# Optimization experiments

Hardware: AMD Instinct MI355X
Metric: run time of the kernel (lower is better)

Reference implementation:

```python
import jax, jax.numpy as jnp
import numpy as np

NUM_NODES = 50000
NUM_EDGES = 800000
NUM_REL = 8
DIM = 64
NUM_BLOCKS = 8


def setup_inputs() -> dict:
    key = jax.random.key(0)
    ks = jax.random.split(key, 6)
    x = jax.random.normal(ks[0], (NUM_NODES, DIM), dtype=jnp.float32)
    source = jax.random.randint(ks[1], (NUM_EDGES,), 0, NUM_NODES)
    target = jax.random.randint(ks[2], (NUM_EDGES,), 0, NUM_NODES)
    edge_type = jax.random.randint(ks[3], (NUM_EDGES,), 0, NUM_REL)
    edge_weights = jax.random.uniform(ks[4], (NUM_EDGES,), dtype=jnp.float32)
    bs = DIM // NUM_BLOCKS
    # xavier_normal_ for (bs, bs) blocks: std = sqrt(2 / (fan_in + fan_out))
    std = (2.0 / (bs + bs)) ** 0.5
    blocks = std * jax.random.normal(ks[5], (NUM_REL, NUM_BLOCKS, bs, bs), dtype=jnp.float32)
    return {
        "x": x,
        "blocks": blocks,
        "edge_weights": edge_weights,
        "source": source,
        "target": target,
        "edge_type": edge_type,
    }


def reference(x, blocks, edge_weights, source, target, edge_type):
    # input_dim == output_dim -> use_horizontal_stacking is False -> vertically stacked path.
    # Vertically stacked adjacency: adj[(edge_type * N + target), source] = edge_weights,
    # so (adj @ x) is a per-(relation,target) scatter-add of weighted source features.
    n = x.shape[0]
    r, b, ib, ob = blocks.shape
    seg = edge_type * n + target                               # (E,) row index in stacked adj
    msgs = x[source] * edge_weights[:, None]                   # (E, in_dim)
    agg = jax.ops.segment_sum(msgs, seg, num_segments=r * n)   # (R*N, in_dim)
    agg = agg.reshape(r, n, b, ib)                             # (R, N, B, ib)
    out = jnp.einsum("rbio,rnbi->nbo", blocks, agg)            # sum over relations + block matmul
    return out.reshape(n, b * ob)                              # (N, out_dim)
```

## Files before the change

kernel.cpp:

```cpp
#include <hip/hip_runtime.h>


#define DIM 64
#define NBLK 8
#define BS 8
#define NREL 8
#define COL_PAD 12
#define LDS_T_TOTAL (NREL * NBLK * BS * COL_PAD)
#define CHUNK 64

#define TILE 4096
#define MAXB 1024
#define SORTW_CAP 4096

typedef unsigned int uint32;
typedef unsigned long long uint64;
typedef unsigned short uint16;

__global__ __launch_bounds__(512) void histA(
    const int* __restrict__ tgt, uint32* __restrict__ tile_hist,
    int num_edges, int nb)
{
    __shared__ uint32 h[MAXB];
    for (int i = threadIdx.x; i < nb; i += 512) h[i] = 0u;
    __syncthreads();
    const int base = blockIdx.x * TILE;
    const int end  = min(base + TILE, num_edges);
    for (int j = base + (int)threadIdx.x; j < end; j += 512)
        atomicAdd(&h[tgt[j] >> 6], 1u);
    __syncthreads();
    uint32* dst = tile_hist + (size_t)blockIdx.x * nb;
    for (int i = threadIdx.x; i < nb; i += 512) dst[i] = h[i];
}

__global__ __launch_bounds__(64) void colscan(
    uint32* __restrict__ tile_hist, uint32* __restrict__ totals,
    int nt, int nb)
{
    const int b    = blockIdx.x;
    const int lane = threadIdx.x;
    uint32 carry = 0;
    for (int t0 = 0; t0 < nt; t0 += 64) {
        const int t = t0 + lane;
        uint32 v = (t < nt) ? tile_hist[(size_t)t * nb + b] : 0u;
        uint32 xin = v;
#pragma unroll
        for (int d = 1; d < 64; d <<= 1) {
            uint32 tm = __shfl_up(xin, d, 64);
            if (lane >= d) xin += tm;
        }
        if (t < nt) tile_hist[(size_t)t * nb + b] = carry + xin - v;
        carry += __shfl(xin, 63, 64);
    }
    if (lane == 0) totals[b] = carry;
}

__global__ __launch_bounds__(512) void scan_totals(
    const uint32* __restrict__ totals, uint32* __restrict__ bbase, int nb)
{
    __shared__ uint32 wtot[8];
    const int tid = threadIdx.x, lane = tid & 63, wid = tid >> 6;
    uint32 carry = 0;
    const int nch = (nb + 511) >> 9;
    for (int c = 0; c < nch; ++c) {
        const int idx = (c << 9) + tid;
        uint32 v = (idx < nb) ? totals[idx] : 0u;
        uint32 xin = v;
#pragma unroll
        for (int d = 1; d < 64; d <<= 1) {
            uint32 t = __shfl_up(xin, d, 64);
            if (lane >= d) xin += t;
        }
        if (lane == 63) wtot[wid] = xin;
        __syncthreads();
        if (wid == 0) {
            uint32 y = (lane < 8) ? wtot[lane] : 0u;
#pragma unroll
            for (int d = 1; d < 8; d <<= 1) {
                uint32 t = __shfl_up(y, d, 64);
                if (lane >= d) y += t;
            }
            if (lane < 8) wtot[lane] = y;
        }
        __syncthreads();
        const uint32 base = carry + ((wid > 0) ? wtot[wid - 1] : 0u);
        if (idx < nb) bbase[idx] = base + xin - v;
        carry += wtot[7];
        __syncthreads();
    }
    if (tid == 0) bbase[nb] = carry;
}

__global__ __launch_bounds__(512) void scatterB(
    const int* __restrict__ src, const int* __restrict__ tgt,
    const int* __restrict__ etype, const float* __restrict__ ew,
    const uint32* __restrict__ tile_hist, const uint32* __restrict__ bbase,
    uint64* __restrict__ payload, int num_edges, int nb)
{
    __shared__ uint32 cur[MAXB];
    const uint32* th = tile_hist + (size_t)blockIdx.x * nb;
    for (int i = threadIdx.x; i < nb; i += 512) cur[i] = bbase[i] + th[i];
    __syncthreads();
    const int base = blockIdx.x * TILE;
    const int end  = min(base + TILE, num_edges);
    for (int j = base + (int)threadIdx.x; j < end; j += 512) {
        const int t = tgt[j];
        const uint32 pos = atomicAdd(&cur[t >> 6], 1u);
        const uint32 lo = (uint32)src[j] | ((uint32)etype[j] << 16)
                        | ((uint32)(t & 63) << 19);
        payload[pos] = ((uint64)__float_as_uint(ew[j]) << 32) | lo;
    }
}

__global__ __launch_bounds__(256) void sortW(
    uint64* __restrict__ payload, uint16* __restrict__ keyt,
    const uint32* __restrict__ bbase)
{
    __shared__ uint64 pay[SORTW_CAP];
    __shared__ uint32 hist[64];
    __shared__ uint32 cur[64];
    const int b   = blockIdx.x;
    const int beg = (int)bbase[b];
    const int cnt = (int)bbase[b + 1] - beg;

    if (cnt > SORTW_CAP) {
        for (int k = threadIdx.x; k < cnt; k += 256) {
            const uint32 lo = (uint32)payload[beg + k];
            keyt[beg + k] = (uint16)((b << 6) | ((lo >> 19) & 63u));
        }
        return;
    }

    for (int k = threadIdx.x; k < cnt; k += 256) pay[k] = payload[beg + k];
    if (threadIdx.x < 64) hist[threadIdx.x] = 0u;
    __syncthreads();
    for (int k = threadIdx.x; k < cnt; k += 256)
        atomicAdd(&hist[((uint32)pay[k] >> 19) & 63u], 1u);
    __syncthreads();
    if (threadIdx.x < 64) {
        const int lane = threadIdx.x;
        uint32 v = hist[lane], xin = v;
#pragma unroll
        for (int d = 1; d < 64; d <<= 1) {
            uint32 t = __shfl_up(xin, d, 64);
            if (lane >= d) xin += t;
        }
        cur[lane] = xin - v;
    }
    __syncthreads();
    for (int k = threadIdx.x; k < cnt; k += 256) {
        const uint64 p  = pay[k];
        const uint32 tl = ((uint32)p >> 19) & 63u;
        const uint32 pos = atomicAdd(&cur[tl], 1u);
        payload[beg + pos] = p;
        keyt[beg + pos] = (uint16)((b << 6) | tl);
    }
}

#define PRE(i, p_)                                                          \
    const uint32 lo##i = (uint32)(p_);                                      \
    const float  w##i  = __uint_as_float((uint32)((p_) >> 32));             \
    const float* bp##i = bcol + ((lo##i >> 16) & 7) * (NBLK * BS * COL_PAD);\
    const float4 c0_##i = *(const float4*)bp##i;                            \
    const float4 c1_##i = *(const float4*)(bp##i + 4);                      \
    const float4* xs##i = (const float4*)(x + (size_t)(lo##i & 0xFFFF) * DIM + b * BS); \
    const float4 v0_##i = xs##i[0];                                         \
    const float4 v1_##i = xs##i[1];

#define ACC(i, t_)                                                          \
    {                                                                       \
        const int tt = (int)(t_);                                           \
        if (tt != tcur) {                                                   \
            atomicAdd(out + (size_t)tcur * DIM + lane, acc);                \
            acc = 0.0f; tcur = tt;                                          \
        }                                                                   \
        acc = fmaf(w##i,                                                    \
                   v0_##i.x * c0_##i.x + v0_##i.y * c0_##i.y +              \
                   v0_##i.z * c0_##i.z + v0_##i.w * c0_##i.w +              \
                   v1_##i.x * c1_##i.x + v1_##i.y * c1_##i.y +              \
                   v1_##i.z * c1_##i.z + v1_##i.w * c1_##i.w, acc);         \
    }

__global__ __launch_bounds__(512) void rgcn_chunk_kernel(
    const float* __restrict__ x,
    const float* __restrict__ blocks,
    const uint64* __restrict__ payload,
    const uint16* __restrict__ keyt,
    float* __restrict__ out,
    int num_edges)
{
    __shared__ float blkT[LDS_T_TOTAL];
    for (int l = threadIdx.x; l < NREL * NBLK * BS * BS; l += blockDim.x) {
        const int o = l & 7;
        const int i = (l >> 3) & 7;
        const int rb = l >> 6;
        blkT[(rb * 8 + o) * COL_PAD + i] = blocks[l];
    }
    __syncthreads();

    const int lane = threadIdx.x & 63;
    const int wid  = __builtin_amdgcn_readfirstlane(threadIdx.x >> 6);
    const int wave = blockIdx.x * (int)(blockDim.x >> 6) + wid;
    const int beg  = wave * CHUNK;
    if (beg >= num_edges) return;
    const int end  = min(beg + CHUNK, num_edges);

    const int b  = lane >> 3;
    const int oo = lane & 7;
    const float* bcol = &blkT[(b * 8 + oo) * COL_PAD];

    int   tcur = (int)keyt[beg];
    float acc  = 0.0f;

    int j = beg;
    for (; j + 4 <= end; j += 4) {
        const uint64 p0 = payload[j];
        const uint64 p1 = payload[j + 1];
        const uint64 p2 = payload[j + 2];
        const uint64 p3 = payload[j + 3];
        const ushort4 kk = *(const ushort4*)(keyt + j);
        PRE(0, p0) PRE(1, p1) PRE(2, p2) PRE(3, p3)
        ACC(0, kk.x) ACC(1, kk.y) ACC(2, kk.z) ACC(3, kk.w)
    }
    for (; j < end; ++j) {
        const uint64 p0 = payload[j];
        const uint16 k0 = keyt[j];
        PRE(0, p0)
        ACC(0, k0)
    }
    atomicAdd(out + (size_t)tcur * DIM + lane, acc);
}

#define LDS_BLK_STRIDE 72
#define LDS_REL_STRIDE (NBLK * LDS_BLK_STRIDE)
#define LDS_TOTAL (NREL * LDS_REL_STRIDE)

__global__ __launch_bounds__(256) void rgcn_edge_kernel(
    const float* __restrict__ x, const float* __restrict__ blocks,
    const float* __restrict__ ew, const int* __restrict__ src,
    const int* __restrict__ tgt, const int* __restrict__ etype,
    float* __restrict__ out, int num_edges)
{
    __shared__ float blk[LDS_TOTAL];
    for (int l = threadIdx.x; l < NREL * NBLK * BS * BS; l += blockDim.x) {
        int r = l >> 9, bb = (l >> 6) & 7, rest = l & 63;
        blk[r * LDS_REL_STRIDE + bb * LDS_BLK_STRIDE + rest] = blocks[l];
    }
    __syncthreads();
    const int lane = threadIdx.x & 63;
    const int wave = blockIdx.x * (blockDim.x >> 6) + (threadIdx.x >> 6);
    const int total_waves = gridDim.x * (blockDim.x >> 6);
    const int b = lane >> 3;
    for (int e = wave; e < num_edges; e += total_waves) {
        const int s = src[e], t = tgt[e], r = etype[e];
        const float w = ew[e];
        const float4* xs = reinterpret_cast<const float4*>(x + (size_t)s * DIM + b * BS);
        const float4 v0 = xs[0], v1 = xs[1];
        const float* bb = &blk[r * LDS_REL_STRIDE + b * LDS_BLK_STRIDE + (lane & 7)];
        float a = v0.x * bb[0] + v0.y * bb[BS] + v0.z * bb[2 * BS] + v0.w * bb[3 * BS]
                + v1.x * bb[4 * BS] + v1.y * bb[5 * BS] + v1.z * bb[6 * BS] + v1.w * bb[7 * BS];
        atomicAdd(&out[(size_t)t * DIM + lane], w * a);
    }
}

extern "C" void kernel_launch(void* const* d_in, const int* in_sizes, int n_in,
                              void* d_out, int out_size, void* d_ws, size_t ws_size,
                              hipStream_t stream) {
    const float* x      = (const float*)d_in[0];
    const float* blocks = (const float*)d_in[1];
    const float* ew     = (const float*)d_in[2];
    const int*   src    = (const int*)d_in[3];
    const int*   tgt    = (const int*)d_in[4];
    const int*   etype  = (const int*)d_in[5];
    float* out = (float*)d_out;

    const int num_edges = in_sizes[2];
    const int num_nodes = in_sizes[0] / DIM;

    const int nb = (num_nodes + 63) >> 6;
    const int nt = (num_edges + TILE - 1) / TILE;

    const size_t payload_b = (size_t)num_edges * 8;
    const size_t keyt_b    = (size_t)num_edges * 2;
    const size_t th_b      = (size_t)nt * nb * 4;
    const size_t tot_b     = (size_t)nb * 4;
    const size_t bb_b      = (size_t)(nb + 1) * 4;
    const size_t need      = payload_b + keyt_b + th_b + tot_b + bb_b;

    if (nb > MAXB || ws_size < need) {
        hipMemsetAsync(d_out, 0, (size_t)out_size * sizeof(float), stream);
        rgcn_edge_kernel<<<2048, 256, 0, stream>>>(
            x, blocks, ew, src, tgt, etype, out, num_edges);
        return;
    }

    char* ws = (char*)d_ws;
    uint64* payload   = (uint64*)ws;
    uint16* keyt      = (uint16*)(ws + payload_b);
    uint32* tile_hist = (uint32*)(ws + payload_b + keyt_b);
    uint32* totals    = (uint32*)(ws + payload_b + keyt_b + th_b);
    uint32* bbase     = (uint32*)(ws + payload_b + keyt_b + th_b + tot_b);

    hipMemsetAsync(d_out, 0, (size_t)out_size * sizeof(float), stream);
    histA<<<nt, 512, 0, stream>>>(tgt, tile_hist, num_edges, nb);
    colscan<<<nb, 64, 0, stream>>>(tile_hist, totals, nt, nb);
    scan_totals<<<1, 512, 0, stream>>>(totals, bbase, nb);
    scatterB<<<nt, 512, 0, stream>>>(
        src, tgt, etype, ew, tile_hist, bbase, payload, num_edges, nb);
    sortW<<<nb, 256, 0, stream>>>(payload, keyt, bbase);

    const int waves   = (num_edges + CHUNK - 1) / CHUNK;
    const int gblocks = (waves + 7) / 8;
    rgcn_chunk_kernel<<<gblocks, 512, 0, stream>>>(
        x, blocks, payload, keyt, out, num_edges);
}
```

Measured before the change: 103.0 us.

## Fuse bucket sort into compute kernel and use global atomic histogram

```diff
diff --git a/kernel.cpp b/kernel.cpp
--- a/kernel.cpp
+++ b/kernel.cpp
@@ -7,18 +7,17 @@
 #define NREL 8
 #define COL_PAD 12
 #define LDS_T_TOTAL (NREL * NBLK * BS * COL_PAD)
-#define CHUNK 64
 
 #define TILE 4096
 #define MAXB 1024
-#define SORTW_CAP 4096
+#define SORT_CAP 2048
+#define NW 8
 
 typedef unsigned int uint32;
 typedef unsigned long long uint64;
-typedef unsigned short uint16;
-
-__global__ __launch_bounds__(512) void histA(
-    const int* __restrict__ tgt, uint32* __restrict__ tile_hist,
+
+__global__ __launch_bounds__(512) void hist_kernel(
+    const int* __restrict__ tgt, uint32* __restrict__ ghist,
     int num_edges, int nb)
 {
     __shared__ uint32 h[MAXB];
@@ -29,34 +28,13 @@
     for (int j = base + (int)threadIdx.x; j < end; j += 512)
         atomicAdd(&h[tgt[j] >> 6], 1u);
     __syncthreads();
-    uint32* dst = tile_hist + (size_t)blockIdx.x * nb;
-    for (int i = threadIdx.x; i < nb; i += 512) dst[i] = h[i];
-}
-
-__global__ __launch_bounds__(64) void colscan(
-    uint32* __restrict__ tile_hist, uint32* __restrict__ totals,
-    int nt, int nb)
-{
-    const int b    = blockIdx.x;
-    const int lane = threadIdx.x;
-    uint32 carry = 0;
-    for (int t0 = 0; t0 < nt; t0 += 64) {
-        const int t = t0 + lane;
-        uint32 v = (t < nt) ? tile_hist[(size_t)t * nb + b] : 0u;
-        uint32 xin = v;
-#pragma unroll
-        for (int d = 1; d < 64; d <<= 1) {
-            uint32 tm = __shfl_up(xin, d, 64);
-            if (lane >= d) xin += tm;
-        }
-        if (t < nt) tile_hist[(size_t)t * nb + b] = carry + xin - v;
-        carry += __shfl(xin, 63, 64);
-    }
-    if (lane == 0) totals[b] = carry;
-}
-
-__global__ __launch_bounds__(512) void scan_totals(
-    const uint32* __restrict__ totals, uint32* __restrict__ bbase, int nb)
+    for (int i = threadIdx.x; i < nb; i += 512)
+        if (h[i]) atomicAdd(&ghist[i], h[i]);
+}
+
+__global__ __launch_bounds__(512) void scan_kernel(
+    const uint32* __restrict__ ghist, uint32* __restrict__ bbase,
+    uint32* __restrict__ gcur, int nb)
 {
     __shared__ uint32 wtot[8];
     const int tid = threadIdx.x, lane = tid & 63, wid = tid >> 6;
@@ -64,7 +42,7 @@
     const int nch = (nb + 511) >> 9;
     for (int c = 0; c < nch; ++c) {
         const int idx = (c << 9) + tid;
-        uint32 v = (idx < nb) ? totals[idx] : 0u;
+        uint32 v = (idx < nb) ? ghist[idx] : 0u;
         uint32 xin = v;
 #pragma unroll
         for (int d = 1; d < 64; d <<= 1) {
@@ -84,25 +62,35 @@
         }
         __syncthreads();
         const uint32 base = carry + ((wid > 0) ? wtot[wid - 1] : 0u);
-        if (idx < nb) bbase[idx] = base + xin - v;
+        if (idx < nb) {
+            const uint32 e = base + xin - v;
+            bbase[idx] = e;
+            gcur[idx]  = e;
+        }
         carry += wtot[7];
         __syncthreads();
     }
     if (tid == 0) bbase[nb] = carry;
 }
 
-__global__ __launch_bounds__(512) void scatterB(
+__global__ __launch_bounds__(512) void scatterG(
     const int* __restrict__ src, const int* __restrict__ tgt,
     const int* __restrict__ etype, const float* __restrict__ ew,
-    const uint32* __restrict__ tile_hist, const uint32* __restrict__ bbase,
-    uint64* __restrict__ payload, int num_edges, int nb)
-{
+    uint32* __restrict__ gcur, uint64* __restrict__ payload,
+    int num_edges, int nb)
+{
+    __shared__ uint32 h[MAXB];
     __shared__ uint32 cur[MAXB];
-    const uint32* th = tile_hist + (size_t)blockIdx.x * nb;
-    for (int i = threadIdx.x; i < nb; i += 512) cur[i] = bbase[i] + th[i];
+    for (int i = threadIdx.x; i < nb; i += 512) h[i] = 0u;
     __syncthreads();
     const int base = blockIdx.x * TILE;
     const int end  = min(base + TILE, num_edges);
+    for (int j = base + (int)threadIdx.x; j < end; j += 512)
+        atomicAdd(&h[tgt[j] >> 6], 1u);
+    __syncthreads();
+    for (int i = threadIdx.x; i < nb; i += 512)
+        if (h[i]) cur[i] = atomicAdd(&gcur[i], h[i]);
+    __syncthreads();
     for (int j = base + (int)threadIdx.x; j < end; j += 512) {
         const int t = tgt[j];
         const uint32 pos = atomicAdd(&cur[t >> 6], 1u);
@@ -112,66 +100,21 @@
     }
 }
 
-__global__ __launch_bounds__(256) void sortW(
-    uint64* __restrict__ payload, uint16* __restrict__ keyt,
-    const uint32* __restrict__ bbase)
-{
-    __shared__ uint64 pay[SORTW_CAP];
-    __shared__ uint32 hist[64];
-    __shared__ uint32 cur[64];
-    const int b   = blockIdx.x;
-    const int beg = (int)bbase[b];
-    const int cnt = (int)bbase[b + 1] - beg;
-
-    if (cnt > SORTW_CAP) {
-        for (int k = threadIdx.x; k < cnt; k += 256) {
-            const uint32 lo = (uint32)payload[beg + k];
-            keyt[beg + k] = (uint16)((b << 6) | ((lo >> 19) & 63u));
-        }
-        return;
-    }
-
-    for (int k = threadIdx.x; k < cnt; k += 256) pay[k] = payload[beg + k];
-    if (threadIdx.x < 64) hist[threadIdx.x] = 0u;
-    __syncthreads();
-    for (int k = threadIdx.x; k < cnt; k += 256)
-        atomicAdd(&hist[((uint32)pay[k] >> 19) & 63u], 1u);
-    __syncthreads();
-    if (threadIdx.x < 64) {
-        const int lane = threadIdx.x;
-        uint32 v = hist[lane], xin = v;
-#pragma unroll
-        for (int d = 1; d < 64; d <<= 1) {
-            uint32 t = __shfl_up(xin, d, 64);
-            if (lane >= d) xin += t;
-        }
-        cur[lane] = xin - v;
-    }
-    __syncthreads();
-    for (int k = threadIdx.x; k < cnt; k += 256) {
-        const uint64 p  = pay[k];
-        const uint32 tl = ((uint32)p >> 19) & 63u;
-        const uint32 pos = atomicAdd(&cur[tl], 1u);
-        payload[beg + pos] = p;
-        keyt[beg + pos] = (uint16)((b << 6) | tl);
-    }
-}
-
 #define PRE(i, p_)                                                          \
     const uint32 lo##i = (uint32)(p_);                                      \
     const float  w##i  = __uint_as_float((uint32)((p_) >> 32));             \
     const float* bp##i = bcol + ((lo##i >> 16) & 7) * (NBLK * BS * COL_PAD);\
     const float4 c0_##i = *(const float4*)bp##i;                            \
     const float4 c1_##i = *(const float4*)(bp##i + 4);                      \
-    const float4* xs##i = (const float4*)(x + (size_t)(lo##i & 0xFFFF) * DIM + b * BS); \
+    const float4* xs##i = (const float4*)(x + (size_t)(lo##i & 0xFFFF) * DIM + bq * BS); \
     const float4 v0_##i = xs##i[0];                                         \
     const float4 v1_##i = xs##i[1];
 
-#define ACC(i, t_)                                                          \
+#define ACC(i)                                                              \
     {                                                                       \
-        const int tt = (int)(t_);                                           \
+        const int tt = (int)((lo##i >> 19) & 63u);                          \
         if (tt != tcur) {                                                   \
-            atomicAdd(out + (size_t)tcur * DIM + lane, acc);                \
+            atomicAdd(out + ((size_t)(n0 + tcur)) * DIM + lane, acc);       \
             acc = 0.0f; tcur = tt;                                          \
         }                                                                   \
         acc = fmaf(w##i,                                                    \
@@ -181,54 +124,89 @@
                    v1_##i.z * c1_##i.z + v1_##i.w * c1_##i.w, acc);         \
     }
 
-__global__ __launch_bounds__(512) void rgcn_chunk_kernel(
+__global__ __launch_bounds__(512) void rgcn_bucket_kernel(
     const float* __restrict__ x,
     const float* __restrict__ blocks,
     const uint64* __restrict__ payload,
-    const uint16* __restrict__ keyt,
+    const uint32* __restrict__ bbase,
     float* __restrict__ out,
-    int num_edges)
-{
-    __shared__ float blkT[LDS_T_TOTAL];
-    for (int l = threadIdx.x; l < NREL * NBLK * BS * BS; l += blockDim.x) {
+    int num_nodes)
+{
+    __shared__ float  blkT[LDS_T_TOTAL];
+    __shared__ uint64 pay[SORT_CAP];
+    __shared__ uint32 hist[64];
+    __shared__ uint32 cur[64];
+
+    const int bkt = blockIdx.x;
+    const int beg = (int)bbase[bkt];
+    const int cnt = (int)bbase[bkt + 1] - beg;
+    if (cnt == 0) return;
+
+    for (int l = threadIdx.x; l < NREL * NBLK * BS * BS; l += 512) {
         const int o = l & 7;
         const int i = (l >> 3) & 7;
         const int rb = l >> 6;
         blkT[(rb * 8 + o) * COL_PAD + i] = blocks[l];
     }
+
+    const bool sorted = (cnt <= SORT_CAP);
+    if (sorted) {
+        if (threadIdx.x < 64) hist[threadIdx.x] = 0u;
+        __syncthreads();
+        const uint32* plo = (const uint32*)(payload + beg);
+        for (int k = threadIdx.x; k < cnt; k += 512)
+            atomicAdd(&hist[(plo[2 * k] >> 19) & 63u], 1u);
+        __syncthreads();
+        if (threadIdx.x < 64) {
+            const int lane = threadIdx.x;
+            uint32 v = hist[lane], xin = v;
+#pragma unroll
+            for (int d = 1; d < 64; d <<= 1) {
+                uint32 t = __shfl_up(xin, d, 64);
+                if (lane >= d) xin += t;
+            }
+            cur[lane] = xin - v;
+        }
+        __syncthreads();
+        for (int k = threadIdx.x; k < cnt; k += 512) {
+            const uint64 p = payload[beg + k];
+            const uint32 tl = ((uint32)p >> 19) & 63u;
+            pay[atomicAdd(&cur[tl], 1u)] = p;
+        }
+    }
     __syncthreads();
 
     const int lane = threadIdx.x & 63;
-    const int wid  = __builtin_amdgcn_readfirstlane(threadIdx.x >> 6);
-    const int wave = blockIdx.x * (int)(blockDim.x >> 6) + wid;
-    const int beg  = wave * CHUNK;
-    if (beg >= num_edges) return;
-    const int end  = min(beg + CHUNK, num_edges);
-
-    const int b  = lane >> 3;
-    const int oo = lane & 7;
-    const float* bcol = &blkT[(b * 8 + oo) * COL_PAD];
-
-    int   tcur = (int)keyt[beg];
-    float acc  = 0.0f;
-
-    int j = beg;
-    for (; j + 4 <= end; j += 4) {
-        const uint64 p0 = payload[j];
-        const uint64 p1 = payload[j + 1];
-        const uint64 p2 = payload[j + 2];
-        const uint64 p3 = payload[j + 3];
-        const ushort4 kk = *(const ushort4*)(keyt + j);
-        PRE(0, p0) PRE(1, p1) PRE(2, p2) PRE(3, p3)
-        ACC(0, kk.x) ACC(1, kk.y) ACC(2, kk.z) ACC(3, kk.w)
-    }
-    for (; j < end; ++j) {
-        const uint64 p0 = payload[j];
-        const uint16 k0 = keyt[j];
-        PRE(0, p0)
-        ACC(0, k0)
-    }
-    atomicAdd(out + (size_t)tcur * DIM + lane, acc);
+    const int wid  = __builtin_amdgcn_readfirstlane((int)threadIdx.x >> 6);
+    const int bq   = lane >> 3;
+    const int oo   = lane & 7;
+    const float* bcol = &blkT[(bq * 8 + oo) * COL_PAD];
+    const int n0 = bkt << 6;
+
+    const uint64* ep = sorted ? (const uint64*)pay : payload + beg;
+
+    const int nch = (cnt + 63) >> 6;
+    for (int c = wid; c < nch; c += NW) {
+        const int s0 = c << 6;
+        const int s1 = min(s0 + 64, cnt);
+        int   tcur = (int)(((uint32)ep[s0] >> 19) & 63u);
+        float acc  = 0.0f;
+        int j = s0;
+        for (; j + 4 <= s1; j += 4) {
+            const uint64 p0 = ep[j];
+            const uint64 p1 = ep[j + 1];
+            const uint64 p2 = ep[j + 2];
+            const uint64 p3 = ep[j + 3];
+            PRE(0, p0) PRE(1, p1) PRE(2, p2) PRE(3, p3)
+            ACC(0) ACC(1) ACC(2) ACC(3)
+        }
+        for (; j < s1; ++j) {
+            const uint64 p0 = ep[j];
+            PRE(0, p0)
+            ACC(0)
+        }
+        atomicAdd(out + ((size_t)(n0 + tcur)) * DIM + lane, acc);
+    }
 }
 
 #define LDS_BLK_STRIDE 72
@@ -281,11 +259,10 @@
     const int nt = (num_edges + TILE - 1) / TILE;
 
     const size_t payload_b = (size_t)num_edges * 8;
-    const size_t keyt_b    = (size_t)num_edges * 2;
-    const size_t th_b      = (size_t)nt * nb * 4;
-    const size_t tot_b     = (size_t)nb * 4;
+    const size_t gh_b      = (size_t)nb * 4;
     const size_t bb_b      = (size_t)(nb + 1) * 4;
-    const size_t need      = payload_b + keyt_b + th_b + tot_b + bb_b;
+    const size_t gc_b      = (size_t)nb * 4;
+    const size_t need      = payload_b + gh_b + bb_b + gc_b;
 
     if (nb > MAXB || ws_size < need) {
         hipMemsetAsync(d_out, 0, (size_t)out_size * sizeof(float), stream);
@@ -295,22 +272,17 @@
     }
 
     char* ws = (char*)d_ws;
-    uint64* payload   = (uint64*)ws;
-    uint16* keyt      = (uint16*)(ws + payload_b);
-    uint32* tile_hist = (uint32*)(ws + payload_b + keyt_b);
-    uint32* totals    = (uint32*)(ws + payload_b + keyt_b + th_b);
-    uint32* bbase     = (uint32*)(ws + payload_b + keyt_b + th_b + tot_b);
-
+    uint64* payload = (uint64*)ws;
+    uint32* ghist   = (uint32*)(ws + payload_b);
+    uint32* bbase   = (uint32*)(ws + payload_b + gh_b);
+    uint32* gcur    = (uint32*)(ws + payload_b + gh_b + bb_b);
+
+    hipMemsetAsync(ghist, 0, gh_b, stream);
     hipMemsetAsync(d_out, 0, (size_t)out_size * sizeof(float), stream);
-    histA<<<nt, 512, 0, stream>>>(tgt, tile_hist, num_edges, nb);
-    colscan<<<nb, 64, 0, stream>>>(tile_hist, totals, nt, nb);
-    scan_totals<<<1, 512, 0, stream>>>(totals, bbase, nb);
-    scatterB<<<nt, 512, 0, stream>>>(
-        src, tgt, etype, ew, tile_hist, bbase, payload, num_edges, nb);
-    sortW<<<nb, 256, 0, stream>>>(payload, keyt, bbase);
-
-    const int waves   = (num_edges + CHUNK - 1) / CHUNK;
-    const int gblocks = (waves + 7) / 8;
-    rgcn_chunk_kernel<<<gblocks, 512, 0, stream>>>(
-        x, blocks, payload, keyt, out, num_edges);
-}
+    hist_kernel<<<nt, 512, 0, stream>>>(tgt, ghist, num_edges, nb);
+    scan_kernel<<<1, 512, 0, stream>>>(ghist, bbase, gcur, nb);
+    scatterG<<<nt, 512, 0, stream>>>(
+        src, tgt, etype, ew, gcur, payload, num_edges, nb);
+    rgcn_bucket_kernel<<<nb, 512, 0, stream>>>(
+        x, blocks, payload, bbase, out, num_nodes);
+}
```

Measured after the change: 125.5 us. 1.22x slower.

## Aggregate per (target,relation) before block transform, sort edges by relation too

Applied to the files above, without the earlier changes.

```diff
diff --git a/kernel.cpp b/kernel.cpp
--- a/kernel.cpp
+++ b/kernel.cpp
@@ -112,73 +112,100 @@
     }
 }
 
-__global__ __launch_bounds__(256) void sortW(
+__global__ __launch_bounds__(512) void sortW(
     uint64* __restrict__ payload, uint16* __restrict__ keyt,
     const uint32* __restrict__ bbase)
 {
     __shared__ uint64 pay[SORTW_CAP];
-    __shared__ uint32 hist[64];
-    __shared__ uint32 cur[64];
+    __shared__ uint32 hist[512];
+    __shared__ uint32 cur[512];
+    __shared__ uint32 wtot[8];
+    const int tid = threadIdx.x;
     const int b   = blockIdx.x;
     const int beg = (int)bbase[b];
     const int cnt = (int)bbase[b + 1] - beg;
 
     if (cnt > SORTW_CAP) {
-        for (int k = threadIdx.x; k < cnt; k += 256) {
+        for (int k = tid; k < cnt; k += 512) {
             const uint32 lo = (uint32)payload[beg + k];
             keyt[beg + k] = (uint16)((b << 6) | ((lo >> 19) & 63u));
         }
         return;
     }
 
-    for (int k = threadIdx.x; k < cnt; k += 256) pay[k] = payload[beg + k];
-    if (threadIdx.x < 64) hist[threadIdx.x] = 0u;
-    __syncthreads();
-    for (int k = threadIdx.x; k < cnt; k += 256)
-        atomicAdd(&hist[((uint32)pay[k] >> 19) & 63u], 1u);
-    __syncthreads();
-    if (threadIdx.x < 64) {
-        const int lane = threadIdx.x;
-        uint32 v = hist[lane], xin = v;
+    for (int k = tid; k < cnt; k += 512) pay[k] = payload[beg + k];
+    hist[tid] = 0u;
+    __syncthreads();
+    for (int k = tid; k < cnt; k += 512)
+        atomicAdd(&hist[((uint32)pay[k] >> 16) & 511u], 1u);
+    __syncthreads();
+    {
+        const int lane = tid & 63, wid = tid >> 6;
+        uint32 v = hist[tid], xin = v;
 #pragma unroll
         for (int d = 1; d < 64; d <<= 1) {
             uint32 t = __shfl_up(xin, d, 64);
             if (lane >= d) xin += t;
         }
-        cur[lane] = xin - v;
-    }
-    __syncthreads();
-    for (int k = threadIdx.x; k < cnt; k += 256) {
-        const uint64 p  = pay[k];
-        const uint32 tl = ((uint32)p >> 19) & 63u;
-        const uint32 pos = atomicAdd(&cur[tl], 1u);
+        if (lane == 63) wtot[wid] = xin;
+        __syncthreads();
+        if (wid == 0) {
+            uint32 y = (lane < 8) ? wtot[lane] : 0u;
+#pragma unroll
+            for (int d = 1; d < 8; d <<= 1) {
+                uint32 t = __shfl_up(y, d, 64);
+                if (lane >= d) y += t;
+            }
+            if (lane < 8) wtot[lane] = y;
+        }
+        __syncthreads();
+        cur[tid] = ((wid > 0) ? wtot[wid - 1] : 0u) + xin - v;
+    }
+    __syncthreads();
+    for (int k = tid; k < cnt; k += 512) {
+        const uint64 p   = pay[k];
+        const uint32 key = ((uint32)p >> 16) & 511u;
+        const uint32 pos = atomicAdd(&cur[key], 1u);
         payload[beg + pos] = p;
-        keyt[beg + pos] = (uint16)((b << 6) | tl);
-    }
-}
-
-#define PRE(i, p_)                                                          \
-    const uint32 lo##i = (uint32)(p_);                                      \
-    const float  w##i  = __uint_as_float((uint32)((p_) >> 32));             \
-    const float* bp##i = bcol + ((lo##i >> 16) & 7) * (NBLK * BS * COL_PAD);\
-    const float4 c0_##i = *(const float4*)bp##i;                            \
-    const float4 c1_##i = *(const float4*)(bp##i + 4);                      \
-    const float4* xs##i = (const float4*)(x + (size_t)(lo##i & 0xFFFF) * DIM + b * BS); \
-    const float4 v0_##i = xs##i[0];                                         \
-    const float4 v1_##i = xs##i[1];
+        keyt[beg + pos] = (uint16)((b << 6) | (key >> 3));
+    }
+}
+
+#define XFORM(r_)                                                           \
+    {                                                                       \
+        const float* bp = bcol + (int)(r_) * (NBLK * BS * COL_PAD);         \
+        const float4 c0 = *(const float4*)bp;                               \
+        const float4 c1 = *(const float4*)(bp + 4);                         \
+        const int bl = lane & ~7;                                           \
+        oacc += c0.x * __shfl(agg, bl + 0, 64)                              \
+              + c0.y * __shfl(agg, bl + 1, 64)                              \
+              + c0.z * __shfl(agg, bl + 2, 64)                              \
+              + c0.w * __shfl(agg, bl + 3, 64)                              \
+              + c1.x * __shfl(agg, bl + 4, 64)                              \
+              + c1.y * __shfl(agg, bl + 5, 64)                              \
+              + c1.z * __shfl(agg, bl + 6, 64)                              \
+              + c1.w * __shfl(agg, bl + 7, 64);                             \
+        agg = 0.0f;                                                         \
+    }
+
+#define PREQ(i, lov, wv)                                                    \
+    const uint32 lo##i = (lov);                                             \
+    const float  w##i  = __uint_as_float(wv);                               \
+    const float  xv##i = x[((size_t)(lo##i & 0xFFFFu) << 6) + lane];
 
 #define ACC(i, t_)                                                          \
     {                                                                       \
-        const int tt = (int)(t_);                                           \
-        if (tt != tcur) {                                                   \
-            atomicAdd(out + (size_t)tcur * DIM + lane, acc);                \
-            acc = 0.0f; tcur = tt;                                          \
+        const int    tt = (int)(t_);                                        \
+        const uint32 rr = (lo##i >> 16) & 7u;                               \
+        if (tt != tcur || rr != rcur) {                                     \
+            XFORM(rcur)                                                     \
+            if (tt != tcur) {                                               \
+                atomicAdd(out + (size_t)tcur * DIM + lane, oacc);           \
+                oacc = 0.0f; tcur = tt;                                     \
+            }                                                               \
+            rcur = rr;                                                      \
         }                                                                   \
-        acc = fmaf(w##i,                                                    \
-                   v0_##i.x * c0_##i.x + v0_##i.y * c0_##i.y +              \
-                   v0_##i.z * c0_##i.z + v0_##i.w * c0_##i.w +              \
-                   v1_##i.x * c1_##i.x + v1_##i.y * c1_##i.y +              \
-                   v1_##i.z * c1_##i.z + v1_##i.w * c1_##i.w, acc);         \
+        agg = fmaf(w##i, xv##i, agg);                                       \
     }
 
 __global__ __launch_bounds__(512) void rgcn_chunk_kernel(
@@ -205,30 +232,38 @@
     if (beg >= num_edges) return;
     const int end  = min(beg + CHUNK, num_edges);
 
-    const int b  = lane >> 3;
+    const int bq = lane >> 3;
     const int oo = lane & 7;
-    const float* bcol = &blkT[(b * 8 + oo) * COL_PAD];
-
-    int   tcur = (int)keyt[beg];
-    float acc  = 0.0f;
+    const float* bcol = &blkT[(bq * 8 + oo) * COL_PAD];
+
+    int    tcur = (int)keyt[beg];
+    uint32 rcur = ((uint32)payload[beg] >> 16) & 7u;
+    float  agg  = 0.0f;
+    float  oacc = 0.0f;
 
     int j = beg;
-    for (; j + 4 <= end; j += 4) {
-        const uint64 p0 = payload[j];
-        const uint64 p1 = payload[j + 1];
-        const uint64 p2 = payload[j + 2];
-        const uint64 p3 = payload[j + 3];
-        const ushort4 kk = *(const ushort4*)(keyt + j);
-        PRE(0, p0) PRE(1, p1) PRE(2, p2) PRE(3, p3)
-        ACC(0, kk.x) ACC(1, kk.y) ACC(2, kk.z) ACC(3, kk.w)
+    for (; j + 8 <= end; j += 8) {
+        const uint4 q0 = *(const uint4*)(payload + j);
+        const uint4 q1 = *(const uint4*)(payload + j + 2);
+        const uint4 q2 = *(const uint4*)(payload + j + 4);
+        const uint4 q3 = *(const uint4*)(payload + j + 6);
+        const ushort4 ka = *(const ushort4*)(keyt + j);
+        const ushort4 kb = *(const ushort4*)(keyt + j + 4);
+        PREQ(0, q0.x, q0.y) PREQ(1, q0.z, q0.w)
+        PREQ(2, q1.x, q1.y) PREQ(3, q1.z, q1.w)
+        PREQ(4, q2.x, q2.y) PREQ(5, q2.z, q2.w)
+        PREQ(6, q3.x, q3.y) PREQ(7, q3.z, q3.w)
+        ACC(0, ka.x) ACC(1, ka.y) ACC(2, ka.z) ACC(3, ka.w)
+        ACC(4, kb.x) ACC(5, kb.y) ACC(6, kb.z) ACC(7, kb.w)
     }
     for (; j < end; ++j) {
         const uint64 p0 = payload[j];
         const uint16 k0 = keyt[j];
-        PRE(0, p0)
+        PREQ(0, (uint32)p0, (uint32)(p0 >> 32))
         ACC(0, k0)
     }
-    atomicAdd(out + (size_t)tcur * DIM + lane, acc);
+    XFORM(rcur)
+    atomicAdd(out + (size_t)tcur * DIM + lane, oacc);
 }
 
 #define LDS_BLK_STRIDE 72
@@ -307,7 +342,7 @@
     scan_totals<<<1, 512, 0, stream>>>(totals, bbase, nb);
     scatterB<<<nt, 512, 0, stream>>>(
         src, tgt, etype, ew, tile_hist, bbase, payload, num_edges, nb);
-    sortW<<<nb, 256, 0, stream>>>(payload, keyt, bbase);
+    sortW<<<nb, 512, 0, stream>>>(payload, keyt, bbase);
 
     const int waves   = (num_edges + CHUNK - 1) / CHUNK;
     const int gblocks = (waves + 7) / 8;
```

After: 91.08 us. -11.6%, faster.
